# Optimization experiments

Hardware: AMD Instinct MI355X
Metric: run time of the kernel (lower is better)

Reference implementation:

```python
import jax, jax.numpy as jnp
import numpy as np

B, SQ, SK = 2, 2048, 2048
QDIM = KDIM = HID = 1024
H = 16
DH = HID // H  # inner_dim = 64


def setup_inputs() -> dict:
    key = jax.random.key(0)
    ks = jax.random.split(key, 8)
    q = jax.random.normal(ks[0], (B, SQ, QDIM), dtype=jnp.float32)
    k = jax.random.normal(ks[1], (B, SK, KDIM), dtype=jnp.float32)
    v = jax.random.normal(ks[2], (B, SK, KDIM), dtype=jnp.float32)
    mask = jax.random.randint(ks[3], (B, SQ, SK), 0, 2).astype(jnp.bool_)
    scale = 1.0 / np.sqrt(QDIM)
    # per-head projections, stored stacked: [H, in_dim, DH]
    Wq = jax.random.normal(ks[4], (H, QDIM, DH), dtype=jnp.float32) * scale
    Wk = jax.random.normal(ks[5], (H, KDIM, DH), dtype=jnp.float32) * scale
    Wv = jax.random.normal(ks[6], (H, KDIM, DH), dtype=jnp.float32) * scale
    Wo = jax.random.normal(ks[7], (HID, QDIM), dtype=jnp.float32) * scale
    return {"q": q, "k": k, "v": v, "mask": mask,
            "Wq": Wq, "Wk": Wk, "Wv": Wv, "Wo": Wo}


def reference(q, k, v, mask, Wq, Wk, Wv, Wo):
    dh = Wq.shape[-1]
    qh = jnp.einsum('bsd,hde->bhse', q, Wq)   # [B,H,SQ,DH]
    kh = jnp.einsum('bsd,hde->bhse', k, Wk)   # [B,H,SK,DH]
    vh = jnp.einsum('bsd,hde->bhse', v, Wv)   # [B,H,SK,DH]
    scores = jnp.einsum('bhqd,bhkd->bhqk', qh, kh) / jnp.sqrt(jnp.asarray(dh, qh.dtype))
    scores = jnp.where(mask[:, None, :, :], -jnp.inf, scores)
    attn = jax.nn.softmax(scores, axis=-1)
    att = jnp.einsum('bhqk,bhkd->bhqd', attn, vh)        # [B,H,SQ,DH]
    concat = att.transpose(0, 2, 1, 3).reshape(q.shape[0], q.shape[1], -1)  # head-order concat
    return concat @ Wo  # [B,SQ,QDIM]
```

## Files before the change

kernel.cpp:

```cpp
#include <hip/hip_runtime.h>

#define NB 2
#define NH 16
#define SEQ 2048
#define DMODEL 1024
#define DHEAD 64
#define QSCALE 0.18033688f

typedef __attribute__((ext_vector_type(8))) short bf16x8;
typedef __attribute__((ext_vector_type(4))) short bf16x4;
typedef __attribute__((ext_vector_type(4))) float f32x4;
typedef __attribute__((ext_vector_type(16))) float f32x16;
typedef __attribute__((ext_vector_type(4))) int i32x4;

static __device__ __forceinline__ unsigned short f2bf(float f) {
    unsigned int u = __float_as_uint(f);
    u += 0x7fffu + ((u >> 16) & 1u);
    return (unsigned short)(u >> 16);
}
static __device__ __forceinline__ unsigned int pk2(float lo, float hi) {
    return (unsigned int)f2bf(lo) | ((unsigned int)f2bf(hi) << 16);
}
static __device__ __forceinline__ void gld_lds16(const unsigned short* g, unsigned short* l) {
    __builtin_amdgcn_global_load_lds(
        (const __attribute__((address_space(1))) unsigned int*)g,
        (__attribute__((address_space(3))) unsigned int*)l, 16, 0, 0);
}

__global__ __launch_bounds__(256) void prep_kernel(
    const int* __restrict__ mask, unsigned long long* __restrict__ mpack,
    const float* __restrict__ Wq, const float* __restrict__ Wk, const float* __restrict__ Wv,
    unsigned short* __restrict__ Wqt, unsigned short* __restrict__ Wkt,
    unsigned short* __restrict__ Wvt,
    const float* __restrict__ Wo, unsigned short* __restrict__ Wot,
    const float* __restrict__ q, const float* __restrict__ k, const float* __restrict__ v,
    unsigned short* __restrict__ qb, unsigned short* __restrict__ kb,
    unsigned short* __restrict__ vb)
{
    __shared__ __align__(16) float Ls[64][65];
    const int bid = blockIdx.x, t = threadIdx.x;

    if (bid < 1024) {
        const int wave = bid * 4 + (t >> 6);
        const int lane = t & 63;
        const int* row = mask + (size_t)wave * SEQ;
        unsigned long long* orow = mpack + (size_t)wave * (SEQ / 64);
        for (int w = 0; w < SEQ / 64; ++w) {
            int m = row[w * 64 + lane];
            unsigned long long bits = __ballot(m != 0);
            if (lane == 0) orow[w] = bits;
        }
    } else if (bid < 2048) {
        const float* S; unsigned short* D; float scale; int R, tile_r, tile_c, ostride;
        if (bid < 1792) {
            const int local = bid - 1024, z = local >> 4, sel = z >> 4, h = z & 15;
            S = (sel == 0 ? Wq : sel == 1 ? Wk : Wv) + (size_t)h * DMODEL * DHEAD;
            D = (sel == 0 ? Wqt : sel == 1 ? Wkt : Wvt) + (size_t)h * DMODEL * DHEAD;
            scale = (sel == 0) ? QSCALE : 1.0f;
            tile_r = (local & 15) * 64; tile_c = 0; R = DHEAD; ostride = DMODEL;
        } else {
            const int local = bid - 1792;
            S = Wo; D = Wot; scale = 1.0f;
            tile_c = (local & 15) * 64; tile_r = (local >> 4) * 64; R = DMODEL; ostride = DMODEL;
        }
        const int c4 = (t & 15) * 4;
        for (int rr = t >> 4; rr < 64; rr += 16) {
            float4 x = *(const float4*)(S + (size_t)(tile_r + rr) * R + tile_c + c4);
            Ls[rr][c4 + 0] = x.x; Ls[rr][c4 + 1] = x.y;
            Ls[rr][c4 + 2] = x.z; Ls[rr][c4 + 3] = x.w;
        }
        __syncthreads();
        const int r4 = (t & 15) * 4;
        for (int cc = t >> 4; cc < 64; cc += 16) {
            ushort4 o;
            o.x = f2bf(Ls[r4 + 0][cc] * scale); o.y = f2bf(Ls[r4 + 1][cc] * scale);
            o.z = f2bf(Ls[r4 + 2][cc] * scale); o.w = f2bf(Ls[r4 + 3][cc] * scale);
            *(ushort4*)(D + (size_t)(tile_c + cc) * ostride + tile_r + r4) = o;
        }
    } else {
        const int local = bid - 2048;
        const int z = local >> 11;
        const float* S = (z == 0) ? q : (z == 1) ? k : v;
        unsigned short* D = (z == 0) ? qb : (z == 1) ? kb : vb;
        const size_t i = ((size_t)(local & 2047) * 256 + t) * 8;
        float4 x0 = *(const float4*)(S + i);
        float4 x1 = *(const float4*)(S + i + 4);
        uint4 val;
        val.x = pk2(x0.x, x0.y); val.y = pk2(x0.z, x0.w);
        val.z = pk2(x1.x, x1.y); val.w = pk2(x1.z, x1.w);
        *(uint4*)(D + i) = val;
    }
}

__global__ __launch_bounds__(256) void proj_gemm_kernel(
    const unsigned short* __restrict__ qb, const unsigned short* __restrict__ kb,
    const unsigned short* __restrict__ vb,
    const unsigned short* __restrict__ Wqt, const unsigned short* __restrict__ Wkt,
    const unsigned short* __restrict__ Wvt,
    unsigned short* __restrict__ qh, unsigned short* __restrict__ kh,
    unsigned short* __restrict__ vt)
{
    const int bid = blockIdx.x;
    const int sx = bid >> 3;
    const int mtg = (bid & 7) * 12 + (sx >> 3);
    const int z = mtg >> 5;
    const int m0 = (mtg & 31) * 128;
    const int n0 = (sx & 7) * 128;

    const unsigned short* A = (z == 0) ? qb : (z == 1) ? kb : vb;
    const unsigned short* Bt = (z == 0) ? Wqt : (z == 1) ? Wkt : Wvt;

    const int t = threadIdx.x, lane = t & 63, w = t >> 6;
    const int lg = lane >> 4, ln = lane & 15;
    const int wx = w & 1, wy = w >> 1;

    __shared__ __align__(16) unsigned short As[128 * 64];
    __shared__ __align__(16) unsigned short Bs[128 * 64];

    f32x4 acc[4][4] = {};

    for (int kk = 0; kk < DMODEL; kk += 64) {
        #pragma unroll
        for (int i = 0; i < 4; ++i) {
            int s = (w * 4 + i) * 64 + lane;
            int n = s >> 3, c = (s & 7) ^ (n & 7);
            gld_lds16(Bt + (size_t)(n0 + n) * DMODEL + kk + c * 8, Bs + (size_t)s * 8);
        }
        #pragma unroll
        for (int i = 0; i < 4; ++i) {
            int s = (w * 4 + i) * 64 + lane;
            int n = s >> 3, c = (s & 7) ^ (n & 7);
            gld_lds16(A + (size_t)(m0 + n) * DMODEL + kk + c * 8, As + (size_t)s * 8);
        }
        __syncthreads();
        #pragma unroll
        for (int ks = 0; ks < 2; ++ks) {
            bf16x8 af[4], bf[4];
            #pragma unroll
            for (int rb = 0; rb < 4; ++rb) {
                int r = wy * 64 + rb * 16 + ln;
                af[rb] = *(const bf16x8*)(As + r * 64 + (((ks * 4 + lg) ^ (r & 7)) * 8));
            }
            #pragma unroll
            for (int nb = 0; nb < 4; ++nb) {
                int n = wx * 64 + nb * 16 + ln;
                bf[nb] = *(const bf16x8*)(Bs + n * 64 + (((ks * 4 + lg) ^ (n & 7)) * 8));
            }
            #pragma unroll
            for (int rb = 0; rb < 4; ++rb)
                #pragma unroll
                for (int nb = 0; nb < 4; ++nb)
                    acc[rb][nb] = __builtin_amdgcn_mfma_f32_16x16x32_bf16(
                        af[rb], bf[nb], acc[rb][nb], 0, 0, 0);
        }
        __syncthreads();
    }

    if (z < 2) {
        unsigned short* Y = (z == 0) ? qh : kh;
        #pragma unroll
        for (int rb = 0; rb < 4; ++rb)
            #pragma unroll
            for (int nb = 0; nb < 4; ++nb)
                #pragma unroll
                for (int r = 0; r < 4; ++r) {
                    int grow = m0 + wy * 64 + rb * 16 + lg * 4 + r;
                    int gcol = n0 + wx * 64 + nb * 16 + ln;
                    size_t idx = ((size_t)((grow >> 11) * NH + (gcol >> 6)) * SEQ
                                  + (grow & (SEQ - 1))) * DHEAD + (gcol & 63);
                    Y[idx] = f2bf(acc[rb][nb][r]);
                }
    } else {
        #pragma unroll
        for (int rb = 0; rb < 4; ++rb)
            #pragma unroll
            for (int nb = 0; nb < 4; ++nb) {
                int grow0 = m0 + wy * 64 + rb * 16 + lg * 4;
                int gcol  = n0 + wx * 64 + nb * 16 + ln;
                int bh = ((grow0 >> 11) << 4) + (gcol >> 6);
                ushort4 st;
                st.x = f2bf(acc[rb][nb][0]); st.y = f2bf(acc[rb][nb][1]);
                st.z = f2bf(acc[rb][nb][2]); st.w = f2bf(acc[rb][nb][3]);
                *(ushort4*)(vt + ((size_t)bh * DHEAD + (gcol & 63)) * SEQ
                                 + (grow0 & (SEQ - 1))) = st;
            }
    }
}

__global__ __launch_bounds__(256, 4) void attn_kernel(
    const unsigned short* __restrict__ qh, const unsigned short* __restrict__ kh,
    const unsigned short* __restrict__ vt, const unsigned long long* __restrict__ mpack,
    unsigned short* __restrict__ Opart, float* __restrict__ Lpart)
{
    const int t = threadIdx.x, lane = t & 63, w = t >> 6;
    const int h = lane >> 5, lq = lane & 31;
    const int L = lq & 7, X = (lq >> 3) & 3;

    const int bid = blockIdx.x;
    const int r_ = bid >> 3;
    const int bh = (bid & 7) * 4 + (r_ >> 5);
    const int r2 = r_ & 31;
    const int qt = r2 >> 1, half = r2 & 1;
    const int b = bh >> 4;
    const int row0 = qt * 128;
    const int qrow = row0 + w * 32 + lq;
    const int kt0 = half * (SEQ / 2);

    __shared__ __align__(16) unsigned short SMEM[4 * 64 * 64];

    const unsigned short* Kb = kh + (size_t)bh * SEQ * DHEAD;
    const unsigned short* Vb = vt + (size_t)bh * DHEAD * SEQ;

    const unsigned short* Qb = qh + ((size_t)bh * SEQ + qrow) * DHEAD;
    bf16x8 qf[4];
    #pragma unroll
    for (int d = 0; d < 4; ++d) qf[d] = *(const bf16x8*)(Qb + d * 16 + h * 8);

    const unsigned long long* Mb = mpack + ((size_t)b * SEQ + qrow) * (SEQ / 64);

    int oK[2], oV[2], sL[2];
    #pragma unroll
    for (int i = 0; i < 2; ++i) {
        const int s = i * 256 + t;
        const int n = s >> 3, c = (s & 7) ^ (n & 7) ^ ((n >> 3) & 3);
        sL[i] = s * 8;
        oK[i] = n * DHEAD + c * 8;
        oV[i] = n * SEQ + c * 8;
    }

    f32x16 acc[2] = {};
    float lsum = 0.f;

    unsigned long long mw, mwn = 0;

    #pragma unroll
    for (int i = 0; i < 2; ++i)
        gld_lds16(Kb + (size_t)kt0 * DHEAD + oK[i], SMEM + sL[i]);
    #pragma unroll
    for (int i = 0; i < 2; ++i)
        gld_lds16(Vb + (size_t)kt0 + oV[i], SMEM + 2 * 4096 + sL[i]);
    mw = Mb[kt0 >> 6];
    __syncthreads();

    for (int tix = 0; tix < 16; ++tix) {
        const int buf = tix & 1;

        if (tix < 15) {
            const int ktn = kt0 + (tix + 1) * 64;
            unsigned short* Kd = SMEM + (buf ^ 1) * 4096;
            unsigned short* Vd = SMEM + 2 * 4096 + (buf ^ 1) * 4096;
            #pragma unroll
            for (int i = 0; i < 2; ++i)
                gld_lds16(Kb + (size_t)ktn * DHEAD + oK[i], Kd + sL[i]);
            #pragma unroll
            for (int i = 0; i < 2; ++i)
                gld_lds16(Vb + (size_t)ktn + oV[i], Vd + sL[i]);
            mwn = Mb[(kt0 >> 6) + tix + 1];
        }

        const unsigned short* Ksb = SMEM + buf * 4096;
        const unsigned short* Vsb = SMEM + 2 * 4096 + buf * 4096;
        const unsigned long long mh_ = mw >> (h * 4);

        #pragma unroll
        for (int st = 0; st < 2; ++st) {
            f32x16 S = {};
            #pragma unroll
            for (int d = 0; d < 4; ++d) {
                bf16x8 kf = *(const bf16x8*)(Ksb + (st * 32 + lq) * 64
                                             + (((d * 2 + h) ^ L ^ X) * 8));
                S = __builtin_amdgcn_mfma_f32_32x32x16_bf16(kf, qf[d], S, 0, 0, 0);
            }
            const int sb = 32 * st;
            unsigned int pd[8];
            #pragma unroll
            for (int bb = 0; bb < 4; ++bb) {
                float e[4];
                #pragma unroll
                for (int rr = 0; rr < 4; ++rr) {
                    const bool m = (mh_ >> (sb + 8 * bb + rr)) & 1ull;
                    float ex = __builtin_amdgcn_exp2f(S[bb * 4 + rr]);
                    e[rr] = m ? 0.0f : ex;
                }
                unsigned int t01 = __builtin_amdgcn_perm(
                    __float_as_uint(e[1]), __float_as_uint(e[0]), 0x07060302u);
                unsigned int t23 = __builtin_amdgcn_perm(
                    __float_as_uint(e[3]), __float_as_uint(e[2]), 0x07060302u);
                lsum += __uint_as_float(t01 << 16);
                lsum += __uint_as_float(t01 & 0xffff0000u);
                lsum += __uint_as_float(t23 << 16);
                lsum += __uint_as_float(t23 & 0xffff0000u);
                pd[bb * 2 + 0] = t01;
                pd[bb * 2 + 1] = t23;
            }
            #pragma unroll
            for (int k2 = 0; k2 < 2; ++k2) {
                i32x4 pi = { (int)pd[4 * k2 + 0], (int)pd[4 * k2 + 1],
                             (int)pd[4 * k2 + 2], (int)pd[4 * k2 + 3] };
                bf16x8 pf = __builtin_bit_cast(bf16x8, pi);
                const int p0 = (((4 * st + 2 * k2) ^ L ^ X)) * 8;
                #pragma unroll
                for (int dt = 0; dt < 2; ++dt) {
                    const unsigned short* vb_ = Vsb + (dt * 32 + lq) * 64 + 4 * h;
                    bf16x4 v0 = *(const bf16x4*)(vb_ + p0);
                    bf16x4 v1 = *(const bf16x4*)(vb_ + (p0 ^ 8));
                    bf16x8 vf = __builtin_shufflevector(v0, v1, 0, 1, 2, 3, 4, 5, 6, 7);
                    acc[dt] = __builtin_amdgcn_mfma_f32_32x32x16_bf16(vf, pf, acc[dt], 0, 0, 0);
                }
            }
        }

        mw = mwn;
        __syncthreads();
    }

    lsum += __shfl_xor(lsum, 32, 64);

    const int OST = 136;
    unsigned short* Osh = SMEM;
    #pragma unroll
    for (int dt = 0; dt < 2; ++dt)
        #pragma unroll
        for (int i = 0; i < 16; ++i) {
            const int dh = dt * 32 + (i & 3) + 8 * (i >> 2) + 4 * h;
            Osh[dh * OST + w * 32 + lq] = f2bf(acc[dt][i]);
        }
    __syncthreads();

    unsigned short* Op = Opart + (size_t)((half << 5) | bh) * DHEAD * SEQ;
    {
        const int dh = t >> 2;
        const int q0 = (t & 3) * 8;
        #pragma unroll
        for (int j = 0; j < 4; ++j) {
            bf16x8 o = *(const bf16x8*)(Osh + dh * OST + q0 + j * 32);
            __builtin_nontemporal_store(
                o, (bf16x8*)(Op + (size_t)dh * SEQ + row0 + q0 + j * 32));
        }
    }
    if (h == 0)
        __builtin_nontemporal_store(lsum, Lpart + (size_t)((half << 5) | bh) * SEQ + qrow);
}

__global__ __launch_bounds__(256) void combine_kernel(
    const unsigned short* __restrict__ Opart, const float* __restrict__ Lpart,
    unsigned short* __restrict__ att)
{
    const int bid = blockIdx.x;
    const int bh = bid >> 4, qt = bid & 15;
    const int b = bh >> 4, hd = bh & 15;
    const int row0 = qt * 128;
    const int t = threadIdx.x;

    __shared__ float linv[128];
    __shared__ unsigned short Ot[128][68];

    if (t < 128) {
        float l = Lpart[(size_t)bh * SEQ + row0 + t]
                + Lpart[(size_t)(32 + bh) * SEQ + row0 + t];
        linv[t] = 1.0f / l;
    }
    __syncthreads();

    const int dh = t >> 2, qg = (t & 3) * 32;
    const unsigned short* p0 = Opart + ((size_t)bh * DHEAD + dh) * SEQ + row0 + qg;
    const unsigned short* p1 = Opart + ((size_t)(32 + bh) * DHEAD + dh) * SEQ + row0 + qg;
    #pragma unroll
    for (int j = 0; j < 4; ++j) {
        uint4 a = *(const uint4*)(p0 + j * 8);
        uint4 c = *(const uint4*)(p1 + j * 8);
        const unsigned int* au = (const unsigned int*)&a;
        const unsigned int* cu = (const unsigned int*)&c;
        #pragma unroll
        for (int d = 0; d < 4; ++d) {
            const int q = qg + j * 8 + d * 2;
            float a0 = __uint_as_float(au[d] << 16);
            float a1 = __uint_as_float(au[d] & 0xffff0000u);
            float c0 = __uint_as_float(cu[d] << 16);
            float c1 = __uint_as_float(cu[d] & 0xffff0000u);
            Ot[q + 0][dh] = f2bf((a0 + c0) * linv[q + 0]);
            Ot[q + 1][dh] = f2bf((a1 + c1) * linv[q + 1]);
        }
    }
    __syncthreads();
    {
        const int q = t >> 1, hf = t & 1;
        const unsigned short* src = &Ot[q][hf * 32];
        unsigned short* dst = att + ((size_t)b * SEQ + row0 + q) * DMODEL
                                  + hd * DHEAD + hf * 32;
        #pragma unroll
        for (int i = 0; i < 8; ++i)
            *(ushort4*)(dst + i * 4) = *(const ushort4*)(src + i * 4);
    }
}

__global__ __launch_bounds__(256) void out_gemm_kernel(
    const unsigned short* __restrict__ A, const unsigned short* __restrict__ Bt,
    float* __restrict__ C)
{
    const int bid = blockIdx.x;
    const int sx = bid >> 3;
    const int m0 = ((bid & 7) * 4 + (sx >> 3)) * 128;
    const int n0 = (sx & 7) * 128;

    const int t = threadIdx.x, lane = t & 63, w = t >> 6;
    const int lg = lane >> 4, ln = lane & 15;
    const int wx = w & 1, wy = w >> 1;

    __shared__ __align__(16) unsigned short As[128 * 64];
    __shared__ __align__(16) unsigned short Bs[128 * 64];

    f32x4 acc[4][4] = {};

    for (int kk = 0; kk < DMODEL; kk += 64) {
        #pragma unroll
        for (int i = 0; i < 4; ++i) {
            int s = (w * 4 + i) * 64 + lane;
            int n = s >> 3, c = (s & 7) ^ (n & 7);
            gld_lds16(Bt + (size_t)(n0 + n) * DMODEL + kk + c * 8, Bs + (size_t)s * 8);
        }
        #pragma unroll
        for (int i = 0; i < 4; ++i) {
            int s = (w * 4 + i) * 64 + lane;
            int n = s >> 3, c = (s & 7) ^ (n & 7);
            gld_lds16(A + (size_t)(m0 + n) * DMODEL + kk + c * 8, As + (size_t)s * 8);
        }
        __syncthreads();
        #pragma unroll
        for (int ks = 0; ks < 2; ++ks) {
            bf16x8 af[4], bf[4];
            #pragma unroll
            for (int rb = 0; rb < 4; ++rb) {
                int r = wy * 64 + rb * 16 + ln;
                af[rb] = *(const bf16x8*)(As + r * 64 + (((ks * 4 + lg) ^ (r & 7)) * 8));
            }
            #pragma unroll
            for (int nb = 0; nb < 4; ++nb) {
                int n = wx * 64 + nb * 16 + ln;
                bf[nb] = *(const bf16x8*)(Bs + n * 64 + (((ks * 4 + lg) ^ (n & 7)) * 8));
            }
            #pragma unroll
            for (int rb = 0; rb < 4; ++rb)
                #pragma unroll
                for (int nb = 0; nb < 4; ++nb)
                    acc[rb][nb] = __builtin_amdgcn_mfma_f32_16x16x32_bf16(
                        af[rb], bf[nb], acc[rb][nb], 0, 0, 0);
        }
        __syncthreads();
    }

    #pragma unroll
    for (int rb = 0; rb < 4; ++rb)
        #pragma unroll
        for (int nb = 0; nb < 4; ++nb)
            #pragma unroll
            for (int r = 0; r < 4; ++r) {
                int grow = m0 + wy * 64 + rb * 16 + lg * 4 + r;
                int gcol = n0 + wx * 64 + nb * 16 + ln;
                C[(size_t)grow * DMODEL + gcol] = acc[rb][nb][r];
            }
}

extern "C" void kernel_launch(void* const* d_in, const int* in_sizes, int n_in,
                              void* d_out, int out_size, void* d_ws, size_t ws_size,
                              hipStream_t stream) {
    const float* q    = (const float*)d_in[0];
    const float* k    = (const float*)d_in[1];
    const float* v    = (const float*)d_in[2];
    const int*   mask = (const int*)  d_in[3];
    const float* Wq   = (const float*)d_in[4];
    const float* Wk   = (const float*)d_in[5];
    const float* Wv   = (const float*)d_in[6];
    const float* Wo   = (const float*)d_in[7];
    float* out = (float*)d_out;

    unsigned short* ws  = (unsigned short*)d_ws;
    const size_t n1 = (size_t)NB * NH * SEQ * DHEAD;
    const size_t nw = (size_t)NH * DHEAD * DMODEL;
    unsigned short* qh  = ws;
    unsigned short* kh  = qh + n1;
    unsigned short* vt  = kh + n1;
    unsigned short* att = vt + n1;
    unsigned short* Wqt = att + n1;
    unsigned short* Wkt = Wqt + nw;
    unsigned short* Wvt = Wkt + nw;
    unsigned short* Wot = Wvt + nw;
    unsigned long long* mpack = (unsigned long long*)(Wot + nw);
    unsigned short* regA = (unsigned short*)(mpack + (size_t)NB * SEQ * (SEQ / 64));
    unsigned short* qb = regA;
    unsigned short* kb = qb + n1;
    unsigned short* vb = kb + n1;
    unsigned short* Opart = regA;
    float* Lpart = (float*)(Opart + (size_t)2 * 32 * DHEAD * SEQ);

    prep_kernel<<<dim3(8192), 256, 0, stream>>>(
        mask, mpack, Wq, Wk, Wv, Wqt, Wkt, Wvt, Wo, Wot, q, k, v, qb, kb, vb);
    proj_gemm_kernel<<<dim3(768), 256, 0, stream>>>(qb, kb, vb, Wqt, Wkt, Wvt, qh, kh, vt);
    attn_kernel<<<dim3(1024), 256, 0, stream>>>(qh, kh, vt, mpack, Opart, Lpart);
    combine_kernel<<<dim3(512), 256, 0, stream>>>(Opart, Lpart, att);
    out_gemm_kernel<<<dim3(256), 256, 0, stream>>>(att, Wot, out);
}
```

Measured before the change: 263.5 us.

## Drop split-K attention and combine kernel; compute row sums via MFMA

Each attention block now walks the full key sequence instead of half, so the separate combine kernel and its partial output and row-sum buffers are no longer needed. The kernel normalises and writes directly into the head-concat attention buffer. The scalar per-element row-sum adds are replaced by an extra MFMA against a ones vector. The grid is halved to 512 blocks with longer loops, which lowers parallelism and tail balance, and launch bounds are relaxed to 2 waves per SIMD.

```diff
diff --git a/kernel.cpp b/kernel.cpp
--- a/kernel.cpp
+++ b/kernel.cpp
@@ -187,10 +187,10 @@
     }
 }
 
-__global__ __launch_bounds__(256, 4) void attn_kernel(
+__global__ __launch_bounds__(256, 2) void attn_kernel(
     const unsigned short* __restrict__ qh, const unsigned short* __restrict__ kh,
     const unsigned short* __restrict__ vt, const unsigned long long* __restrict__ mpack,
-    unsigned short* __restrict__ Opart, float* __restrict__ Lpart)
+    unsigned short* __restrict__ att)
 {
     const int t = threadIdx.x, lane = t & 63, w = t >> 6;
     const int h = lane >> 5, lq = lane & 31;
@@ -198,13 +198,11 @@
 
     const int bid = blockIdx.x;
     const int r_ = bid >> 3;
-    const int bh = (bid & 7) * 4 + (r_ >> 5);
-    const int r2 = r_ & 31;
-    const int qt = r2 >> 1, half = r2 & 1;
-    const int b = bh >> 4;
+    const int qt = r_ & 15;
+    const int bh = (bid & 7) * 4 + (r_ >> 4);
+    const int b = bh >> 4, hd = bh & 15;
     const int row0 = qt * 128;
     const int qrow = row0 + w * 32 + lq;
-    const int kt0 = half * (SEQ / 2);
 
     __shared__ __align__(16) unsigned short SMEM[4 * 64 * 64];
 
@@ -229,24 +227,27 @@
     }
 
     f32x16 acc[2] = {};
-    float lsum = 0.f;
+    f32x16 lacc = {};
+    bf16x8 ones;
+    #pragma unroll
+    for (int i = 0; i < 8; ++i) ones[i] = (short)0x3f80;
 
     unsigned long long mw, mwn = 0;
 
     #pragma unroll
     for (int i = 0; i < 2; ++i)
-        gld_lds16(Kb + (size_t)kt0 * DHEAD + oK[i], SMEM + sL[i]);
+        gld_lds16(Kb + oK[i], SMEM + sL[i]);
     #pragma unroll
     for (int i = 0; i < 2; ++i)
-        gld_lds16(Vb + (size_t)kt0 + oV[i], SMEM + 2 * 4096 + sL[i]);
-    mw = Mb[kt0 >> 6];
+        gld_lds16(Vb + oV[i], SMEM + 2 * 4096 + sL[i]);
+    mw = Mb[0];
     __syncthreads();
 
-    for (int tix = 0; tix < 16; ++tix) {
+    for (int tix = 0; tix < 32; ++tix) {
         const int buf = tix & 1;
 
-        if (tix < 15) {
-            const int ktn = kt0 + (tix + 1) * 64;
+        if (tix < 31) {
+            const int ktn = (tix + 1) * 64;
             unsigned short* Kd = SMEM + (buf ^ 1) * 4096;
             unsigned short* Vd = SMEM + 2 * 4096 + (buf ^ 1) * 4096;
             #pragma unroll
@@ -255,7 +256,7 @@
             #pragma unroll
             for (int i = 0; i < 2; ++i)
                 gld_lds16(Vb + (size_t)ktn + oV[i], Vd + sL[i]);
-            mwn = Mb[(kt0 >> 6) + tix + 1];
+            mwn = Mb[tix + 1];
         }
 
         const unsigned short* Ksb = SMEM + buf * 4096;
@@ -282,22 +283,17 @@
                     float ex = __builtin_amdgcn_exp2f(S[bb * 4 + rr]);
                     e[rr] = m ? 0.0f : ex;
                 }
-                unsigned int t01 = __builtin_amdgcn_perm(
+                pd[bb * 2 + 0] = __builtin_amdgcn_perm(
                     __float_as_uint(e[1]), __float_as_uint(e[0]), 0x07060302u);
-                unsigned int t23 = __builtin_amdgcn_perm(
+                pd[bb * 2 + 1] = __builtin_amdgcn_perm(
                     __float_as_uint(e[3]), __float_as_uint(e[2]), 0x07060302u);
-                lsum += __uint_as_float(t01 << 16);
-                lsum += __uint_as_float(t01 & 0xffff0000u);
-                lsum += __uint_as_float(t23 << 16);
-                lsum += __uint_as_float(t23 & 0xffff0000u);
-                pd[bb * 2 + 0] = t01;
-                pd[bb * 2 + 1] = t23;
             }
             #pragma unroll
             for (int k2 = 0; k2 < 2; ++k2) {
                 i32x4 pi = { (int)pd[4 * k2 + 0], (int)pd[4 * k2 + 1],
                              (int)pd[4 * k2 + 2], (int)pd[4 * k2 + 3] };
                 bf16x8 pf = __builtin_bit_cast(bf16x8, pi);
+                lacc = __builtin_amdgcn_mfma_f32_32x32x16_bf16(ones, pf, lacc, 0, 0, 0);
                 const int p0 = (((4 * st + 2 * k2) ^ L ^ X)) * 8;
                 #pragma unroll
                 for (int dt = 0; dt < 2; ++dt) {
@@ -314,84 +310,20 @@
         __syncthreads();
     }
 
-    lsum += __shfl_xor(lsum, 32, 64);
-
-    const int OST = 136;
-    unsigned short* Osh = SMEM;
+    const float linv = 1.0f / lacc[0];
+    unsigned short* Ar = att + ((size_t)b * SEQ + qrow) * DMODEL + hd * DHEAD;
     #pragma unroll
     for (int dt = 0; dt < 2; ++dt)
         #pragma unroll
-        for (int i = 0; i < 16; ++i) {
-            const int dh = dt * 32 + (i & 3) + 8 * (i >> 2) + 4 * h;
-            Osh[dh * OST + w * 32 + lq] = f2bf(acc[dt][i]);
-        }
-    __syncthreads();
-
-    unsigned short* Op = Opart + (size_t)((half << 5) | bh) * DHEAD * SEQ;
-    {
-        const int dh = t >> 2;
-        const int q0 = (t & 3) * 8;
-        #pragma unroll
-        for (int j = 0; j < 4; ++j) {
-            bf16x8 o = *(const bf16x8*)(Osh + dh * OST + q0 + j * 32);
-            __builtin_nontemporal_store(
-                o, (bf16x8*)(Op + (size_t)dh * SEQ + row0 + q0 + j * 32));
-        }
-    }
-    if (h == 0)
-        __builtin_nontemporal_store(lsum, Lpart + (size_t)((half << 5) | bh) * SEQ + qrow);
-}
-
-__global__ __launch_bounds__(256) void combine_kernel(
-    const unsigned short* __restrict__ Opart, const float* __restrict__ Lpart,
-    unsigned short* __restrict__ att)
-{
-    const int bid = blockIdx.x;
-    const int bh = bid >> 4, qt = bid & 15;
-    const int b = bh >> 4, hd = bh & 15;
-    const int row0 = qt * 128;
-    const int t = threadIdx.x;
-
-    __shared__ float linv[128];
-    __shared__ unsigned short Ot[128][68];
-
-    if (t < 128) {
-        float l = Lpart[(size_t)bh * SEQ + row0 + t]
-                + Lpart[(size_t)(32 + bh) * SEQ + row0 + t];
-        linv[t] = 1.0f / l;
-    }
-    __syncthreads();
-
-    const int dh = t >> 2, qg = (t & 3) * 32;
-    const unsigned short* p0 = Opart + ((size_t)bh * DHEAD + dh) * SEQ + row0 + qg;
-    const unsigned short* p1 = Opart + ((size_t)(32 + bh) * DHEAD + dh) * SEQ + row0 + qg;
-    #pragma unroll
-    for (int j = 0; j < 4; ++j) {
-        uint4 a = *(const uint4*)(p0 + j * 8);
-        uint4 c = *(const uint4*)(p1 + j * 8);
-        const unsigned int* au = (const unsigned int*)&a;
-        const unsigned int* cu = (const unsigned int*)&c;
-        #pragma unroll
-        for (int d = 0; d < 4; ++d) {
-            const int q = qg + j * 8 + d * 2;
-            float a0 = __uint_as_float(au[d] << 16);
-            float a1 = __uint_as_float(au[d] & 0xffff0000u);
-            float c0 = __uint_as_float(cu[d] << 16);
-            float c1 = __uint_as_float(cu[d] & 0xffff0000u);
-            Ot[q + 0][dh] = f2bf((a0 + c0) * linv[q + 0]);
-            Ot[q + 1][dh] = f2bf((a1 + c1) * linv[q + 1]);
-        }
-    }
-    __syncthreads();
-    {
-        const int q = t >> 1, hf = t & 1;
-        const unsigned short* src = &Ot[q][hf * 32];
-        unsigned short* dst = att + ((size_t)b * SEQ + row0 + q) * DMODEL
-                                  + hd * DHEAD + hf * 32;
-        #pragma unroll
-        for (int i = 0; i < 8; ++i)
-            *(ushort4*)(dst + i * 4) = *(const ushort4*)(src + i * 4);
-    }
+        for (int g = 0; g < 4; ++g) {
+            const int dh0 = dt * 32 + 8 * g + 4 * h;
+            ushort4 o;
+            o.x = f2bf(acc[dt][g * 4 + 0] * linv);
+            o.y = f2bf(acc[dt][g * 4 + 1] * linv);
+            o.z = f2bf(acc[dt][g * 4 + 2] * linv);
+            o.w = f2bf(acc[dt][g * 4 + 3] * linv);
+            *(ushort4*)(Ar + dh0) = o;
+        }
 }
 
 __global__ __launch_bounds__(256) void out_gemm_kernel(
@@ -490,13 +422,10 @@
     unsigned short* qb = regA;
     unsigned short* kb = qb + n1;
     unsigned short* vb = kb + n1;
-    unsigned short* Opart = regA;
-    float* Lpart = (float*)(Opart + (size_t)2 * 32 * DHEAD * SEQ);
 
     prep_kernel<<<dim3(8192), 256, 0, stream>>>(
         mask, mpack, Wq, Wk, Wv, Wqt, Wkt, Wvt, Wo, Wot, q, k, v, qb, kb, vb);
     proj_gemm_kernel<<<dim3(768), 256, 0, stream>>>(qb, kb, vb, Wqt, Wkt, Wvt, qh, kh, vt);
-    attn_kernel<<<dim3(1024), 256, 0, stream>>>(qh, kh, vt, mpack, Opart, Lpart);
-    combine_kernel<<<dim3(512), 256, 0, stream>>>(Opart, Lpart, att);
+    attn_kernel<<<dim3(512), 256, 0, stream>>>(qh, kh, vt, mpack, att);
     out_gemm_kernel<<<dim3(256), 256, 0, stream>>>(att, Wot, out);
 }
```

Result: no change. 258.7 us (-1.8%).
